# Kernel tuning notes

Hardware: AMD Instinct MI355X
Metric: run time of the kernel (lower is better)

## Reference

```python
import jax, jax.numpy as jnp
import numpy as np

EPS = 1e-5


def layer_norm(x, g, b):
    m = jnp.mean(x, axis=-1, keepdims=True)
    v = jnp.mean((x - m) ** 2, axis=-1, keepdims=True)
    return (x - m) / jnp.sqrt(v + EPS) * g + b


def rel_shift(x, klen):
    # x: [q, p, b, n] -> Transformer-XL relative shift -> [q, klen, b, n]
    q, p, b, n = x.shape
    x = jnp.reshape(x, (p, q, b, n))
    x = x[1:]
    x = jnp.reshape(x, (q, p - 1, b, n))
    return x[:, :klen]


def setup_inputs() -> dict:
    S, B, D, NH, DH, DF = 1024, 4, 1024, 16, 64, 4096
    key = jax.random.key(0)
    ks = jax.random.split(key, 16)
    w = 0.02  # scale random params for numerical sanity
    return {
        "src": jax.random.normal(ks[0], (S, B, D), jnp.float32),
        "pos_emb": jax.random.normal(ks[1], (S + 1, B, D), jnp.float32),
        "src_mask": jnp.zeros((S, S), dtype=bool),
        "qw": jax.random.normal(ks[2], (D, NH, DH), jnp.float32) * w,
        "kw": jax.random.normal(ks[3], (D, NH, DH), jnp.float32) * w,
        "vw": jax.random.normal(ks[4], (D, NH, DH), jnp.float32) * w,
        "rw": jax.random.normal(ks[5], (D, NH, DH), jnp.float32) * w,
        "ow": jax.random.normal(ks[6], (D, NH, DH), jnp.float32) * w,
        "r_w_bias": jax.random.normal(ks[7], (NH, DH), jnp.float32) * w,
        "r_r_bias": jax.random.normal(ks[8], (NH, DH), jnp.float32) * w,
        "w1": jax.random.normal(ks[9], (DF, D), jnp.float32) * w,
        "b1": jnp.zeros((DF,), jnp.float32),
        "w2": jax.random.normal(ks[10], (D, DF), jnp.float32) * w,
        "b2": jnp.zeros((D,), jnp.float32),
        "g1": jnp.ones((D,), jnp.float32),
        "beta1": jnp.zeros((D,), jnp.float32),
        "g2": jnp.ones((D,), jnp.float32),
        "beta2": jnp.zeros((D,), jnp.float32),
    }


def reference(src, pos_emb, src_mask, qw, kw, vw, rw, ow, r_w_bias, r_r_bias,
              w1, b1, w2, b2, g1, beta1, g2, beta2):
    S = src.shape[0]
    d_head = qw.shape[-1]
    scale = 1.0 / d_head ** 0.5

    # mem=None -> cat == src; dropout layers are identity (eval)
    q_head = jnp.einsum('ibh,hnd->ibnd', src, qw)
    k_head = jnp.einsum('ibh,hnd->ibnd', src, kw)
    v_head = jnp.einsum('ibh,hnd->ibnd', src, vw)
    k_pos = jnp.einsum('ibh,hnd->ibnd', pos_emb, rw)

    ac = jnp.einsum('ibnd,jbnd->ijbn', q_head + r_w_bias, k_head)       # [S,S,B,N]
    bd = jnp.einsum('ibnd,jbnd->ijbn', q_head + r_r_bias, k_pos)        # [S,S+1,B,N]
    bd = rel_shift(bd, klen=S)

    mask = src_mask.astype(ac.dtype)[:, :, None, None]
    attn_score = (ac + bd) * scale - 1e30 * mask
    attn_prob = jax.nn.softmax(attn_score, axis=1)

    attn_vec = jnp.einsum('ijbn,jbnd->ibnd', attn_prob, v_head)
    attn_out = jnp.einsum('ibnd,hnd->ibh', attn_vec, ow)

    x = layer_norm(src + attn_out, g1, beta1)
    ff = jax.nn.gelu(x @ w1.T + b1, approximate=False) @ w2.T + b2
    return layer_norm(x + ff, g2, beta2)
```

## Files before the change

### kernel.cpp

```cpp
#include <hip/hip_runtime.h>
#include <math.h>

typedef __bf16 bf16x8 __attribute__((ext_vector_type(8)));
typedef __bf16 bf16x4 __attribute__((ext_vector_type(4)));
typedef float f32x4 __attribute__((ext_vector_type(4)));

__device__ __forceinline__ void gload_lds16(const __bf16* g, __bf16* l) {
  __builtin_amdgcn_global_load_lds((const __attribute__((address_space(1))) void*)g,
                                   (__attribute__((address_space(3))) void*)l, 16, 0, 0);
}

__device__ __forceinline__ float gelu_exact(float v) {
  return 0.5f * v * (1.f + erff(v * 0.70710678118654752f));
}

__global__ __launch_bounds__(256) void prep_all(
    const float* __restrict__ src, __bf16* __restrict__ srcB2,
    const float* __restrict__ pos, __bf16* __restrict__ posB,
    const float* __restrict__ ow, __bf16* __restrict__ owB,
    const float* __restrict__ w1, __bf16* __restrict__ w1B,
    const float* __restrict__ w2, __bf16* __restrict__ w2B,
    const float* __restrict__ qw, const float* __restrict__ kw,
    const float* __restrict__ vw, const float* __restrict__ rw,
    __bf16* __restrict__ qkvT, __bf16* __restrict__ rwT) {
  __shared__ float t[32][33];
  int bid = blockIdx.x;
  const int tid = threadIdx.x;
  if (bid < 4096) {
    const int i = bid & 1023, b = bid >> 10;
    const float4 v = *(const float4*)(src + ((size_t)(i * 4 + b)) * 1024 + tid * 4);
    bf16x4 o = {(__bf16)v.x, (__bf16)v.y, (__bf16)v.z, (__bf16)v.w};
    *(bf16x4*)(srcB2 + (size_t)bid * 1024 + tid * 4) = o;
    return;
  }
  bid -= 4096;
  if (bid < 3329) {
    const float* in; __bf16* out;
    if (bid < 1025) { in = pos; out = posB; }
    else if (bid < 1281) { bid -= 1025; in = ow; out = owB; }
    else if (bid < 2305) { bid -= 1281; in = w1; out = w1B; }
    else { bid -= 2305; in = w2; out = w2B; }
    const int base = bid * 4096 + tid * 4;
#pragma unroll
    for (int k2 = 0; k2 < 4; ++k2) {
      const int off = base + k2 * 1024;
      float4 v = *(const float4*)(in + off);
      bf16x4 o = {(__bf16)v.x, (__bf16)v.y, (__bf16)v.z, (__bf16)v.w};
      *(bf16x4*)(out + off) = o;
    }
    return;
  }
  bid -= 3329;
  const int z = bid >> 10, rem = bid & 1023;
  const float* in; __bf16* out;
  switch (z) {
    case 0: in = qw; out = qkvT; break;
    case 1: in = kw; out = qkvT + 1024 * 1024; break;
    case 2: in = vw; out = qkvT + 2048 * 1024; break;
    default: in = rw; out = rwT; break;
  }
  const int c0 = (rem & 31) * 32, r0 = (rem >> 5) * 32;
  const int tx = tid & 31, ty = tid >> 5;
  for (int yy = ty; yy < 32; yy += 8)
    t[yy][tx] = in[(size_t)(r0 + yy) * 1024 + c0 + tx];
  __syncthreads();
  for (int yy = ty; yy < 32; yy += 8)
    out[(size_t)(c0 + yy) * 1024 + r0 + tx] = (__bf16)t[tx][yy];
}

template<int BM, int BN, int MODE>
__device__ __forceinline__ void gemm_body(
    const __bf16* __restrict__ A, const __bf16* __restrict__ BT,
    float* __restrict__ Cf, __bf16* __restrict__ Cb,
    const float* __restrict__ bias, int M, int N, int K,
    int kStart, int kChunk, int mBase, int nBase, char* smemRaw) {
  constexpr int BK = 32;
  constexpr int ALOAD = (BM * BK) / 2048;
  constexpr int BLOAD = (BN * BK) / 2048;
  __bf16* lA = (__bf16*)smemRaw;
  __bf16* lB = (__bf16*)(smemRaw + 4 * BM * BK);
  const int tid = threadIdx.x;
  const int w = tid >> 6, l = tid & 63;
  const int lr = l & 15, lk = l >> 4;
  const int srow = tid >> 2;
  const int scol = (tid & 3) * 8;
  const int wbase = w * 512;

  const __bf16* aSrc[ALOAD];
  const __bf16* bSrc[BLOAD];
#pragma unroll
  for (int i = 0; i < ALOAD; ++i) {
    int grow = mBase + srow + i * 64;
    grow = grow < M ? grow : M - 1;
    aSrc[i] = A + (size_t)grow * K + kStart + scol;
  }
#pragma unroll
  for (int i = 0; i < BLOAD; ++i) {
    const int grow = nBase + srow + i * 64;
    bSrc[i] = BT + (size_t)grow * K + kStart + scol;
  }
  auto stage = [&](int buf) {
#pragma unroll
    for (int i = 0; i < ALOAD; ++i) {
      gload_lds16(aSrc[i], &lA[buf * BM * BK + i * 2048 + wbase]);
      aSrc[i] += BK;
    }
#pragma unroll
    for (int i = 0; i < BLOAD; ++i) {
      gload_lds16(bSrc[i], &lB[buf * BN * BK + i * 2048 + wbase]);
      bSrc[i] += BK;
    }
  };

  constexpr int WM = BM / 2, WN = BN / 2;
  constexpr int MF = WM / 16, NF = WN / 16;
  const int wr = w >> 1, wc = w & 1;
  f32x4 acc[MF][NF] = {};

  const int nIter = kChunk / BK;
  stage(0);
  int cur = 0;
#pragma unroll 1
  for (int t = 0; t < nIter; ++t) {
    __syncthreads();
    if (t + 1 < nIter) stage(cur ^ 1);
    bf16x8 af[MF], bfr[NF];
#pragma unroll
    for (int mi = 0; mi < MF; ++mi)
      af[mi] = *(const bf16x8*)&lA[cur * BM * BK + (wr * WM + mi * 16 + lr) * BK + lk * 8];
#pragma unroll
    for (int nj = 0; nj < NF; ++nj)
      bfr[nj] = *(const bf16x8*)&lB[cur * BN * BK + (wc * WN + nj * 16 + lr) * BK + lk * 8];
#pragma unroll
    for (int mi = 0; mi < MF; ++mi)
#pragma unroll
      for (int nj = 0; nj < NF; ++nj)
        acc[mi][nj] = __builtin_amdgcn_mfma_f32_16x16x32_bf16(af[mi], bfr[nj], acc[mi][nj], 0, 0, 0);
    cur ^= 1;
  }
#pragma unroll
  for (int mi = 0; mi < MF; ++mi) {
#pragma unroll
    for (int nj = 0; nj < NF; ++nj) {
      const int col = nBase + wc * WN + nj * 16 + lr;
      const int row0 = mBase + wr * WM + mi * 16 + lk * 4;
#pragma unroll
      for (int j = 0; j < 4; ++j) {
        const int row = row0 + j;
        if (row < M) {
          float v = acc[mi][nj][j];
          if constexpr (MODE == 1) {
            v = gelu_exact(v + bias[col]);
            Cb[(size_t)row * N + col] = (__bf16)v;
          } else if constexpr (MODE == 2) {
            Cb[(size_t)row * N + col] = (__bf16)v;
          } else {
            Cf[(size_t)row * N + col] = v;
          }
        }
      }
    }
  }
}

__global__ __launch_bounds__(256)
void proj2_kernel(const __bf16* __restrict__ vwT, const __bf16* __restrict__ srcB2,
                  const __bf16* __restrict__ posB, const __bf16* __restrict__ rwT,
                  __bf16* __restrict__ vTB, __bf16* __restrict__ kposB) {
  __shared__ __align__(16) char smem[4 * (128 + 64) * 32];
  const int raw = blockIdx.x;
  int bid = (raw & 7) * 130 + (raw >> 3);
  if (bid < 512) {
    gemm_body<128, 64, 2>(vwT, srcB2, nullptr, vTB, nullptr, 1024, 4096, 1024,
                          0, 1024, (bid >> 6) * 128, (bid & 63) * 64, smem);
  } else {
    const int t = bid - 512;
    gemm_body<128, 64, 2>(posB, rwT, nullptr, kposB, nullptr, 4100, 1024, 1024,
                          0, 1024, (t >> 4) * 128, (t & 15) * 64, smem);
  }
}

template<int MODE>
__global__ __launch_bounds__(512)
void gemm256(const __bf16* __restrict__ A, const __bf16* __restrict__ BT,
             __bf16* __restrict__ Cb, const float* __restrict__ bias,
             int M, int N, int K) {
  __shared__ __align__(16) __bf16 sm[3 * 24576];
  const int tid = threadIdx.x;
  const int wid = tid >> 6, l = tid & 63;
  const int lcol = l & 15, lk = l >> 4;
  const int wm = wid >> 1, wn = wid & 1;
  const int gx = gridDim.x;
  const int G = gx * gridDim.y;
  const int flat = blockIdx.y * gx + blockIdx.x;
  const int band = G >> 3;
  const int x8 = flat & 7, loc = flat >> 3;
  const int rpb = band / gx;
  const int ny = x8 * rpb + loc % rpb;
  const int nx = loc / rpb;
  const int mBase = ny * 256, nBase = nx * 128;

  int rowj[2], gslotj[2];
#pragma unroll
  for (int j = 0; j < 2; ++j) {
    const int u = (wid * 2 + j) * 64 + l;
    rowj[j] = u >> 3;
    gslotj[j] = (u & 7) ^ (rowj[j] & 7);
  }
  auto issueHT = [&](int kt, int ht, int side) {
    __bf16* base = sm + side * 24576 + (ht == 2 ? 16384 : ht * 8192);
#pragma unroll
    for (int j = 0; j < 2; ++j) {
      const __bf16* src = (ht < 2)
        ? A + (size_t)(mBase + ht * 128 + rowj[j]) * K + kt * 64 + gslotj[j] * 8
        : BT + (size_t)(nBase + rowj[j]) * K + kt * 64 + gslotj[j] * 8;
      gload_lds16(src, base + (wid * 2 + j) * 512);
    }
  };

  const int nkt = K >> 6;
  issueHT(0, 0, 0); issueHT(0, 1, 0); issueHT(0, 2, 0);
  issueHT(1, 0, 1); issueHT(1, 1, 1); issueHT(1, 2, 1);

  f32x4 acc[4][4] = {};
#pragma unroll 1
  for (int j = 0; j < nkt; ++j) {
    asm volatile("s_waitcnt vmcnt(6)" ::: "memory");
    __builtin_amdgcn_s_barrier();
    __builtin_amdgcn_sched_barrier(0);
    const int side = j % 3;
    const int sn = (j + 2) % 3;
    const int ktn = (j + 2 < nkt) ? j + 2 : nkt - 1;
    const __bf16* Ab = sm + side * 24576;
    const __bf16* Bb = Ab + 16384;
    issueHT(ktn, 0, sn);
    bf16x8 af[4][2];
#pragma unroll
    for (int mi = 0; mi < 4; ++mi)
#pragma unroll
      for (int kk = 0; kk < 2; ++kk) {
        const int row = wm * 64 + mi * 16 + lcol;
        af[mi][kk] = *(const bf16x8*)&Ab[row * 64 + (((kk * 4 + lk) ^ (row & 7)) * 8)];
      }
    issueHT(ktn, 1, sn);
    bf16x8 bfv[4][2];
#pragma unroll
    for (int nj = 0; nj < 4; ++nj)
#pragma unroll
      for (int kk = 0; kk < 2; ++kk) {
        const int row = wn * 64 + nj * 16 + lcol;
        bfv[nj][kk] = *(const bf16x8*)&Bb[row * 64 + (((kk * 4 + lk) ^ (row & 7)) * 8)];
      }
    issueHT(ktn, 2, sn);
    __builtin_amdgcn_s_setprio(1);
#pragma unroll
    for (int mi = 0; mi < 4; ++mi)
#pragma unroll
      for (int nj = 0; nj < 4; ++nj) {
        acc[mi][nj] = __builtin_amdgcn_mfma_f32_16x16x32_bf16(af[mi][0], bfv[nj][0], acc[mi][nj], 0, 0, 0);
        acc[mi][nj] = __builtin_amdgcn_mfma_f32_16x16x32_bf16(af[mi][1], bfv[nj][1], acc[mi][nj], 0, 0, 0);
      }
    __builtin_amdgcn_s_setprio(0);
  }
#pragma unroll
  for (int mi = 0; mi < 4; ++mi)
#pragma unroll
    for (int nj = 0; nj < 4; ++nj) {
      const int col = nBase + wn * 64 + nj * 16 + lcol;
      const int row0 = mBase + wm * 64 + mi * 16 + lk * 4;
#pragma unroll
      for (int jj = 0; jj < 4; ++jj) {
        float v = acc[mi][nj][jj];
        if constexpr (MODE == 1) v = gelu_exact(v + bias[col]);
        Cb[(size_t)(row0 + jj) * N + col] = (__bf16)v;
      }
    }
}

template<int MODE>
__global__ __launch_bounds__(512)
void gemm512(const __bf16* __restrict__ A, const __bf16* __restrict__ BT,
             __bf16* __restrict__ Cb0, __bf16* __restrict__ Cb1,
             __bf16* __restrict__ Cb2, __bf16* __restrict__ Cb3,
             const float* __restrict__ bias, int M, int N, int K, int kChunk) {
  __shared__ __align__(16) __bf16 sm[2 * 32768];
  const int tid = threadIdx.x;
  const int w = tid >> 6, l = tid & 63;
  const int lcol = l & 15, lk = l >> 4;
  const int wm = w >> 2, wn = w & 3;
  const int gx = gridDim.x;
  const int G = gx * gridDim.y;
  const int flat = blockIdx.y * gx + blockIdx.x;
  const int band = G >> 3;
  const int x8 = flat & 7, loc = flat >> 3;
  const int rpb = band / gx;
  const int ny = x8 * rpb + loc % rpb;
  const int nx = loc / rpb;
  const int mBase = ny * 256, nBase = nx * 256;
  const int kStart = blockIdx.z * kChunk;
  __bf16* Cb = (blockIdx.z == 0) ? Cb0 : (blockIdx.z == 1) ? Cb1
             : (blockIdx.z == 2) ? Cb2 : Cb3;

  const int rT = tid >> 3;
  const int gslot = ((tid & 7) ^ (rT & 7)) * 8;
  auto stage = [&](int side, int kt) {
#pragma unroll
    for (int i = 0; i < 4; ++i) {
      gload_lds16(A + (size_t)(mBase + i * 64 + rT) * K + kStart + kt * 64 + gslot,
                  sm + side * 32768 + i * 4096 + w * 512);
      gload_lds16(BT + (size_t)(nBase + i * 64 + rT) * K + kStart + kt * 64 + gslot,
                  sm + side * 32768 + 16384 + i * 4096 + w * 512);
    }
  };

  f32x4 acc[8][4] = {};
  const int nIter = kChunk >> 6;
  stage(0, 0);
  int cur = 0;
#pragma unroll 1
  for (int t = 0; t < nIter; ++t) {
    __syncthreads();
    if (t + 1 < nIter) stage(cur ^ 1, t + 1);
    const __bf16* Ab = sm + cur * 32768;
    const __bf16* Bb = Ab + 16384;
    bf16x8 bfv[4][2];
#pragma unroll
    for (int nj = 0; nj < 4; ++nj)
#pragma unroll
      for (int kk = 0; kk < 2; ++kk) {
        const int row = wn * 64 + nj * 16 + lcol;
        bfv[nj][kk] = *(const bf16x8*)&Bb[row * 64 + (((kk * 4 + lk) ^ (row & 7)) * 8)];
      }
    __builtin_amdgcn_s_setprio(1);
#pragma unroll
    for (int mi = 0; mi < 8; ++mi) {
      const int row = wm * 128 + mi * 16 + lcol;
      bf16x8 a0 = *(const bf16x8*)&Ab[row * 64 + ((lk ^ (row & 7)) * 8)];
      bf16x8 a1 = *(const bf16x8*)&Ab[row * 64 + (((4 + lk) ^ (row & 7)) * 8)];
#pragma unroll
      for (int nj = 0; nj < 4; ++nj) {
        acc[mi][nj] = __builtin_amdgcn_mfma_f32_16x16x32_bf16(a0, bfv[nj][0], acc[mi][nj], 0, 0, 0);
        acc[mi][nj] = __builtin_amdgcn_mfma_f32_16x16x32_bf16(a1, bfv[nj][1], acc[mi][nj], 0, 0, 0);
      }
    }
    __builtin_amdgcn_s_setprio(0);
    cur ^= 1;
  }
#pragma unroll
  for (int mi = 0; mi < 8; ++mi)
#pragma unroll
    for (int nj = 0; nj < 4; ++nj) {
      const int col = nBase + wn * 64 + nj * 16 + lcol;
      const int row0 = mBase + wm * 128 + mi * 16 + lk * 4;
#pragma unroll
      for (int jj = 0; jj < 4; ++jj) {
        float v = acc[mi][nj][jj];
        if constexpr (MODE == 1) v = gelu_exact(v + bias[col]);
        Cb[(size_t)(row0 + jj) * N + col] = (__bf16)v;
      }
    }
}

__global__ __launch_bounds__(256)
void attn10(const __bf16* __restrict__ qk, const __bf16* __restrict__ vT,
            const __bf16* __restrict__ kpos, const float* __restrict__ rwbias,
            const float* __restrict__ rrbias, __bf16* __restrict__ av) {
  constexpr float ALPHA = 0.125f * 1.44269504088896f;
  constexpr int PB = 132;
  __shared__ __align__(16) char smem[74240];
  __bf16* sP  = (__bf16*)(smem + 49152);
  __bf16* sbd = (__bf16*)(smem + 57344);

  const int flat = blockIdx.x;
  const int xcd = flat & 7, rr_ = flat >> 3;
  const int bn = xcd * 8 + (rr_ >> 4);
  const int it = rr_ & 15;
  const int b = bn >> 4, n = bn & 15;
  const int i0 = it * 64;
  const int tid = threadIdx.x;
  const int l = tid & 63;
  const int lcol = l & 15, lk = l >> 4;
  const int strip = (tid >> 6) * 16;
  const int wbase = tid & 192;
  const int nh64 = n * 64;
  const int q = strip + lcol;

  const int rB = tid >> 3;
  const int cs8 = ((tid & 7) ^ (rB & 7)) * 8;

  bf16x8 onesf;
#pragma unroll
  for (int u = 0; u < 8; ++u) onesf[u] = (__bf16)1.0f;

  bf16x8 qac[2], qlo[2], qhi[2];
  {
    const __bf16* qrow = qk + ((size_t)(b * 1024 + i0 + q)) * 2048 + nh64;
    int gH = i0 + q + 1; gH = gH < 1024 ? gH : 1023;
    const __bf16* qrowH = qk + ((size_t)(b * 1024 + gH)) * 2048 + nh64;
#pragma unroll
    for (int kk = 0; kk < 2; ++kk) {
      bf16x8 qv = *(const bf16x8*)(qrow + kk * 32 + lk * 8);
      bf16x8 qh = *(const bf16x8*)(qrowH + kk * 32 + lk * 8);
      const int dbase = nh64 + kk * 32 + lk * 8;
#pragma unroll
      for (int u = 0; u < 8; ++u) {
        const float rb = rrbias[dbase + u];
        qac[kk][u] = (__bf16)(((float)qv[u] + rwbias[dbase + u]) * ALPHA);
        qlo[kk][u] = (__bf16)(((float)qv[u] + rb) * ALPHA);
        qhi[kk][u] = (__bf16)(((float)qh[u] + rb) * ALPHA);
      }
    }
  }

#pragma unroll
  for (int kq = 0; kq < 2; ++kq) {
    const int r = kq * 32 + rB;
    const int dst = (kq * 256 + wbase) * 8;
    gload_lds16(kpos + ((size_t)((960 - i0 + r) * 4 + b)) * 1024 + nh64 + cs8,
                (__bf16*)(smem + 40960) + dst);
    gload_lds16(qk + ((size_t)(b * 1024 + r)) * 2048 + 1024 + nh64 + cs8,
                (__bf16*)(smem) + dst);
    const int rrel = r - i0;
    const int idx = (rrel <= 0) ? (1024 + rrel) : (rrel - 1);
    gload_lds16(kpos + ((size_t)(idx * 4 + b)) * 1024 + nh64 + cs8,
                (__bf16*)(smem + 16384) + dst);
    gload_lds16(vT + ((size_t)(nh64 + r)) * 4096 + b * 1024 + cs8,
                (__bf16*)(smem + 32768) + dst);
  }
  __syncthreads();
  {
    __bf16* kpl = (__bf16*)(smem + 40960);
    const int colb0 = (-i0 - 64) & 127;
#pragma unroll
    for (int fb = 0; fb < 4; ++fb) {
      const int row = fb * 16 + lcol;
      f32x4 g = {};
#pragma unroll
      for (int kk = 0; kk < 2; ++kk) {
        bf16x8 a = *(const bf16x8*)&kpl[row * 64 + (((kk * 4 + lk) ^ (lcol & 7)) * 8)];
        g = __builtin_amdgcn_mfma_f32_16x16x32_bf16(a, qlo[kk], g, 0, 0, 0);
      }
      bf16x4 gw = {(__bf16)g[0], (__bf16)g[1], (__bf16)g[2], (__bf16)g[3]};
      *(bf16x4*)&sbd[q * PB + ((colb0 + fb * 16 + lk * 4) & 127)] = gw;
    }
  }
  __syncthreads();

  f32x4 oacc[4] = {};
  f32x4 zq = {};
  size_t kS = (size_t)(b * 1024 + 64 + rB) * 2048 + 1024 + nh64 + cs8;
  size_t vS = (size_t)(nh64 + rB) * 4096 + b * 1024 + 64 + cs8;

  auto jtStep = [&](int jt, const bf16x8 (&qg)[2], bool dofix) {
    const int cur = jt & 1, nxt = cur ^ 1;
    const int d0 = jt * 64 - i0;
    __bf16* sK   = (__bf16*)(smem + cur * 8192);
    __bf16* sKn  = (__bf16*)(smem + nxt * 8192);
    __bf16* sKP  = (__bf16*)(smem + 16384 + cur * 8192);
    __bf16* sKPn = (__bf16*)(smem + 16384 + nxt * 8192);
    __bf16* sVT  = (__bf16*)(smem + 32768 + cur * 8192);
    __bf16* sVTn = (__bf16*)(smem + 32768 + nxt * 8192);
#pragma unroll
    for (int kq = 0; kq < 2; ++kq) {
      const int dst = (kq * 256 + wbase) * 8;
      gload_lds16(qk + kS + kq * 65536, sKn + dst);
      gload_lds16(vT + vS + kq * 131072, sVTn + dst);
      const int rreln = d0 + 64 + kq * 32 + rB;
      const int idx = (rreln <= 0) ? (1024 + rreln) : (rreln - 1);
      gload_lds16(kpos + ((size_t)(idx * 4 + b)) * 1024 + nh64 + cs8, sKPn + dst);
    }
    kS += 131072; vS += 64;
    {
      __builtin_amdgcn_s_setprio(1);
#pragma unroll
      for (int fb = 0; fb < 4; ++fb) {
        const int row = fb * 16 + lcol;
        f32x4 g = {};
        g = __builtin_amdgcn_mfma_f32_16x16x32_bf16(
            *(const bf16x8*)&sKP[row * 64 + ((lk ^ (lcol & 7)) * 8)], qg[0], g, 0, 0, 0);
        g = __builtin_amdgcn_mfma_f32_16x16x32_bf16(
            *(const bf16x8*)&sKP[row * 64 + (((4 + lk) ^ (lcol & 7)) * 8)], qg[1], g, 0, 0, 0);
        bf16x4 gw = {(__bf16)g[0], (__bf16)g[1], (__bf16)g[2], (__bf16)g[3]};
        *(bf16x4*)&sbd[q * PB + ((d0 + fb * 16 + lk * 4) & 127)] = gw;
      }
      __builtin_amdgcn_s_setprio(0);
      if (dofix) {
        const int cl = tid >> 2, part = tid & 3;
        const __bf16* qs = qk + ((size_t)(b * 1024 + i0 + cl)) * 2048 + nh64 + part * 16;
        bf16x8 a0 = *(const bf16x8*)qs;
        bf16x8 a1 = *(const bf16x8*)(qs + 8);
        bf16x8 k0 = *(const bf16x8*)&sKP[(2 * part) * 8];
        bf16x8 k1 = *(const bf16x8*)&sKP[(2 * part + 1) * 8];
        float s64 = 0.f;
#pragma unroll
        for (int u = 0; u < 8; ++u)
          s64 += ((float)a0[u] + rrbias[nh64 + part * 16 + u]) * (float)k0[u]
               + ((float)a1[u] + rrbias[nh64 + part * 16 + 8 + u]) * (float)k1[u];
        s64 += __shfl_xor(s64, 1, 64);
        s64 += __shfl_xor(s64, 2, 64);
        if (part == 0) sbd[cl * PB] = (__bf16)(s64 * ALPHA);
      }
    }
    f32x4 sc[4];
    __builtin_amdgcn_s_setprio(1);
#pragma unroll
    for (int fk = 0; fk < 4; ++fk) {
      const int row = fk * 16 + lcol;
      f32x4 a = {};
#pragma unroll
      for (int kk = 0; kk < 2; ++kk) {
        bf16x8 kf = *(const bf16x8*)&sK[row * 64 + (((kk * 4 + lk) ^ (lcol & 7)) * 8)];
        a = __builtin_amdgcn_mfma_f32_16x16x32_bf16(kf, qac[kk], a, 0, 0, 0);
      }
      sc[fk] = a;
    }
    __builtin_amdgcn_s_setprio(0);
    {
      const int rowb = q * PB;
      const int sb = d0 - q;
#pragma unroll
      for (int fk = 0; fk < 4; ++fk) {
        const int cb = sb + fk * 16 + lk * 4;
        float e0 = exp2f(sc[fk][0] + (float)sbd[rowb + ((cb) & 127)]);
        float e1 = exp2f(sc[fk][1] + (float)sbd[rowb + ((cb + 1) & 127)]);
        float e2 = exp2f(sc[fk][2] + (float)sbd[rowb + ((cb + 2) & 127)]);
        float e3 = exp2f(sc[fk][3] + (float)sbd[rowb + ((cb + 3) & 127)]);
        bf16x4 pw = {(__bf16)e0, (__bf16)e1, (__bf16)e2, (__bf16)e3};
        *(bf16x4*)&sP[q * 64 + (((fk * 2 + (lk >> 1)) ^ (q & 7)) * 8) + (lk & 1) * 4] = pw;
      }
    }
    __builtin_amdgcn_s_setprio(1);
#pragma unroll
    for (int kk = 0; kk < 2; ++kk) {
      bf16x8 pa = *(const bf16x8*)&sP[q * 64 + (((kk * 4 + lk) ^ (q & 7)) * 8)];
      zq = __builtin_amdgcn_mfma_f32_16x16x32_bf16(pa, onesf, zq, 0, 0, 0);
#pragma unroll
      for (int fd = 0; fd < 4; ++fd) {
        const int vrow = fd * 16 + lcol;
        bf16x8 bv = *(const bf16x8*)&sVT[vrow * 64 + (((kk * 4 + lk) ^ (lcol & 7)) * 8)];
        oacc[fd] = __builtin_amdgcn_mfma_f32_16x16x32_bf16(pa, bv, oacc[fd], 0, 0, 0);
      }
    }
    __builtin_amdgcn_s_setprio(0);
    __syncthreads();
  };

#pragma unroll 1
  for (int jt = 0; jt < it; ++jt) jtStep(jt, qlo, false);
  jtStep(it, qhi, true);
#pragma unroll 1
  for (int jt = it + 1; jt < 16; ++jt) jtStep(jt, qhi, false);

#pragma unroll
  for (int jj = 0; jj < 4; ++jj) {
    const float rz = 1.f / zq[jj];
    const int ig = i0 + strip + lk * 4 + jj;
    __bf16* dst = av + ((size_t)(ig * 4 + b)) * 1024 + nh64;
#pragma unroll
    for (int fd = 0; fd < 4; ++fd)
      dst[fd * 16 + lcol] = (__bf16)(oacc[fd][jj] * rz);
  }
}

__global__ __launch_bounds__(256)
void ln_fuse(const float* __restrict__ A, const __bf16* __restrict__ Ab,
             const __bf16* __restrict__ P0, const __bf16* __restrict__ P1,
             const __bf16* __restrict__ P2, const __bf16* __restrict__ P3,
             const float* __restrict__ cb, const float* __restrict__ g,
             const float* __restrict__ be, float* __restrict__ oF,
             __bf16* __restrict__ oB) {
  const int row = blockIdx.x, t = threadIdx.x;
  const size_t base = (size_t)row * 1024 + t * 4;
  float x0, x1, x2, x3;
  if (A) {
    const float4 a = *(const float4*)(A + base);
    x0 = a.x; x1 = a.y; x2 = a.z; x3 = a.w;
  } else {
    const bf16x4 a = *(const bf16x4*)(Ab + base);
    x0 = (float)a[0]; x1 = (float)a[1]; x2 = (float)a[2]; x3 = (float)a[3];
  }
  const bf16x4 p0 = *(const bf16x4*)(P0 + base);
  const bf16x4 p1 = *(const bf16x4*)(P1 + base);
  const bf16x4 p2 = *(const bf16x4*)(P2 + base);
  const bf16x4 p3 = *(const bf16x4*)(P3 + base);
  x0 += (float)p0[0] + (float)p1[0] + (float)p2[0] + (float)p3[0];
  x1 += (float)p0[1] + (float)p1[1] + (float)p2[1] + (float)p3[1];
  x2 += (float)p0[2] + (float)p1[2] + (float)p2[2] + (float)p3[2];
  x3 += (float)p0[3] + (float)p1[3] + (float)p2[3] + (float)p3[3];
  if (cb) {
    const float4 c = *(const float4*)(cb + t * 4);
    x0 += c.x; x1 += c.y; x2 += c.z; x3 += c.w;
  }
  float s = x0 + x1 + x2 + x3;
  float qq = x0 * x0 + x1 * x1 + x2 * x2 + x3 * x3;
#pragma unroll
  for (int o = 1; o < 64; o <<= 1) { s += __shfl_xor(s, o, 64); qq += __shfl_xor(qq, o, 64); }
  __shared__ float ss[4], qs[4];
  if ((t & 63) == 0) { ss[t >> 6] = s; qs[t >> 6] = qq; }
  __syncthreads();
  s = ss[0] + ss[1] + ss[2] + ss[3];
  qq = qs[0] + qs[1] + qs[2] + qs[3];
  const float mean = s * (1.f / 1024.f);
  const float var = qq * (1.f / 1024.f) - mean * mean;
  const float rstd = rsqrtf(var + 1e-5f);
  const float4 gv = *(const float4*)(g + t * 4);
  const float4 bev = *(const float4*)(be + t * 4);
  const float y0 = (x0 - mean) * rstd * gv.x + bev.x;
  const float y1 = (x1 - mean) * rstd * gv.y + bev.y;
  const float y2 = (x2 - mean) * rstd * gv.z + bev.z;
  const float y3 = (x3 - mean) * rstd * gv.w + bev.w;
  if (oF) {
    float4 r = {y0, y1, y2, y3};
    *(float4*)(oF + base) = r;
  }
  if (oB) {
    bf16x4 o4 = {(__bf16)y0, (__bf16)y1, (__bf16)y2, (__bf16)y3};
    *(bf16x4*)(oB + base) = o4;
  }
}

extern "C" void kernel_launch(void* const* d_in, const int* in_sizes, int n_in,
                              void* d_out, int out_size, void* d_ws, size_t ws_size,
                              hipStream_t stream) {
  const float* src    = (const float*)d_in[0];
  const float* pos    = (const float*)d_in[1];
  const float* qw     = (const float*)d_in[3];
  const float* kw     = (const float*)d_in[4];
  const float* vw     = (const float*)d_in[5];
  const float* rw     = (const float*)d_in[6];
  const float* ow     = (const float*)d_in[7];
  const float* rwbias = (const float*)d_in[8];
  const float* rrbias = (const float*)d_in[9];
  const float* w1     = (const float*)d_in[10];
  const float* b1     = (const float*)d_in[11];
  const float* w2     = (const float*)d_in[12];
  const float* b2     = (const float*)d_in[13];
  const float* g1     = (const float*)d_in[14];
  const float* be1    = (const float*)d_in[15];
  const float* g2     = (const float*)d_in[16];
  const float* be2    = (const float*)d_in[17];
  float* out = (float*)d_out;

  char* p = (char*)d_ws;
  auto alloc = [&](size_t bytes) { char* r = p; p += (bytes + 255) & ~(size_t)255; return r; };
  __bf16* qkB   = (__bf16*)alloc(4096ull * 2048 * 2);
  __bf16* vTB   = (__bf16*)alloc(1024ull * 4096 * 2);
  __bf16* kposB = (__bf16*)alloc(4100ull * 1024 * 2);
  __bf16* avB   = (__bf16*)alloc(4096ull * 1024 * 2);
  __bf16* srcB2 = (__bf16*)alloc(4096ull * 1024 * 2);
  __bf16* posB  = (__bf16*)alloc(4100ull * 1024 * 2);
  float*  xF    = (float*)alloc(4096ull * 1024 * 4);
  __bf16* w2B   = (__bf16*)alloc(4096ull * 1024 * 2);
  __bf16* qkvT  = (__bf16*)alloc(3072ull * 1024 * 2);
  __bf16* rwT   = (__bf16*)alloc(1024ull * 1024 * 2);
  __bf16* owB   = (__bf16*)alloc(1024ull * 1024 * 2);
  __bf16* w1B   = (__bf16*)alloc(4096ull * 1024 * 2);
  __bf16* xB    = (__bf16*)alloc(4096ull * 1024 * 2);
  __bf16* gB   = qkB;
  __bf16* xS0  = (__bf16*)xF;
  __bf16* xS1  = (__bf16*)xF + 4194304;

  prep_all<<<11521, 256, 0, stream>>>(src, srcB2, pos, posB, ow, owB, w1, w1B,
                                      w2, w2B, qw, kw, vw, rw, qkvT, rwT);
  gemm256<2><<<dim3(16, 16), 512, 0, stream>>>(srcB2, qkvT, qkB, nullptr, 4096, 2048, 1024);
  proj2_kernel<<<1040, 256, 0, stream>>>(qkvT + 2048 * 1024, srcB2, posB, rwT, vTB, kposB);
  attn10<<<dim3(1024), 256, 0, stream>>>(qkB, vTB, kposB, rwbias, rrbias, avB);
  gemm512<2><<<dim3(4, 16, 4), 512, 0, stream>>>(avB, owB, srcB2, posB, xS0, xS1, nullptr, 4096, 1024, 1024, 256);
  ln_fuse<<<4096, 256, 0, stream>>>(src, nullptr, srcB2, posB, xS0, xS1, nullptr, g1, be1, nullptr, xB);
  gemm512<1><<<dim3(16, 16), 512, 0, stream>>>(xB, w1B, gB, nullptr, nullptr, nullptr, b1, 4096, 4096, 1024, 1024);
  gemm512<2><<<dim3(4, 16, 4), 512, 0, stream>>>(gB, w2B, avB, w1B, xS0, xS1, nullptr, 4096, 1024, 4096, 1024);
  ln_fuse<<<4096, 256, 0, stream>>>(nullptr, xB, avB, w1B, xS0, xS1, b2, g2, be2, out, nullptr);
  (void)in_sizes; (void)n_in; (void)out_size; (void)ws_size;
}
```

Before: 285.2 us.

## Replace double-buffered LDS prefetch in attention with register-staged single buffer

The attention kernel no longer double-buffers its K, positional-K and V^T tiles in LDS using direct global-to-LDS loads. It now prefetches the next tile into registers during the current step, then writes it into a single LDS buffer after an extra barrier. This cuts static LDS from about 74 KB to about 49 KB, which could allow more resident blocks per CU. In exchange it adds a second __syncthreads per iteration, extra VGPR pressure and explicit LDS store instructions.

```diff
diff --git a/kernel.cpp b/kernel.cpp
--- a/kernel.cpp
+++ b/kernel.cpp
@@ -362,14 +362,17 @@
 }
 
 __global__ __launch_bounds__(256)
-void attn10(const __bf16* __restrict__ qk, const __bf16* __restrict__ vT,
+void attn11(const __bf16* __restrict__ qk, const __bf16* __restrict__ vT,
             const __bf16* __restrict__ kpos, const float* __restrict__ rwbias,
             const float* __restrict__ rrbias, __bf16* __restrict__ av) {
   constexpr float ALPHA = 0.125f * 1.44269504088896f;
   constexpr int PB = 132;
-  __shared__ __align__(16) char smem[74240];
-  __bf16* sP  = (__bf16*)(smem + 49152);
-  __bf16* sbd = (__bf16*)(smem + 57344);
+  __shared__ __align__(16) char smem[49664];
+  __bf16* sK  = (__bf16*)(smem);
+  __bf16* sKP = (__bf16*)(smem + 8192);
+  __bf16* sVT = (__bf16*)(smem + 16384);
+  __bf16* sP  = (__bf16*)(smem + 24576);
+  __bf16* sbd = (__bf16*)(smem + 32768);
 
   const int flat = blockIdx.x;
   const int xcd = flat & 7, rr_ = flat >> 3;
@@ -416,20 +419,16 @@
   for (int kq = 0; kq < 2; ++kq) {
     const int r = kq * 32 + rB;
     const int dst = (kq * 256 + wbase) * 8;
-    gload_lds16(kpos + ((size_t)((960 - i0 + r) * 4 + b)) * 1024 + nh64 + cs8,
-                (__bf16*)(smem + 40960) + dst);
-    gload_lds16(qk + ((size_t)(b * 1024 + r)) * 2048 + 1024 + nh64 + cs8,
-                (__bf16*)(smem) + dst);
+    gload_lds16(kpos + ((size_t)((960 - i0 + r) * 4 + b)) * 1024 + nh64 + cs8, sP + dst);
+    gload_lds16(qk + ((size_t)(b * 1024 + r)) * 2048 + 1024 + nh64 + cs8, sK + dst);
     const int rrel = r - i0;
     const int idx = (rrel <= 0) ? (1024 + rrel) : (rrel - 1);
-    gload_lds16(kpos + ((size_t)(idx * 4 + b)) * 1024 + nh64 + cs8,
-                (__bf16*)(smem + 16384) + dst);
-    gload_lds16(vT + ((size_t)(nh64 + r)) * 4096 + b * 1024 + cs8,
-                (__bf16*)(smem + 32768) + dst);
+    gload_lds16(kpos + ((size_t)(idx * 4 + b)) * 1024 + nh64 + cs8, sKP + dst);
+    gload_lds16(vT + ((size_t)(nh64 + r)) * 4096 + b * 1024 + cs8, sVT + dst);
   }
   __syncthreads();
   {
-    __bf16* kpl = (__bf16*)(smem + 40960);
+    const __bf16* kpl = sP;
     const int colb0 = (-i0 - 64) & 127;
 #pragma unroll
     for (int fb = 0; fb < 4; ++fb) {
@@ -452,22 +451,15 @@
   size_t vS = (size_t)(nh64 + rB) * 4096 + b * 1024 + 64 + cs8;
 
   auto jtStep = [&](int jt, const bf16x8 (&qg)[2], bool dofix) {
-    const int cur = jt & 1, nxt = cur ^ 1;
     const int d0 = jt * 64 - i0;
-    __bf16* sK   = (__bf16*)(smem + cur * 8192);
-    __bf16* sKn  = (__bf16*)(smem + nxt * 8192);
-    __bf16* sKP  = (__bf16*)(smem + 16384 + cur * 8192);
-    __bf16* sKPn = (__bf16*)(smem + 16384 + nxt * 8192);
-    __bf16* sVT  = (__bf16*)(smem + 32768 + cur * 8192);
-    __bf16* sVTn = (__bf16*)(smem + 32768 + nxt * 8192);
+    bf16x8 rKr[2], rKPr[2], rVTr[2];
 #pragma unroll
     for (int kq = 0; kq < 2; ++kq) {
-      const int dst = (kq * 256 + wbase) * 8;
-      gload_lds16(qk + kS + kq * 65536, sKn + dst);
-      gload_lds16(vT + vS + kq * 131072, sVTn + dst);
+      rKr[kq] = *(const bf16x8*)(qk + kS + kq * 65536);
+      rVTr[kq] = *(const bf16x8*)(vT + vS + kq * 131072);
       const int rreln = d0 + 64 + kq * 32 + rB;
       const int idx = (rreln <= 0) ? (1024 + rreln) : (rreln - 1);
-      gload_lds16(kpos + ((size_t)(idx * 4 + b)) * 1024 + nh64 + cs8, sKPn + dst);
+      rKPr[kq] = *(const bf16x8*)(kpos + ((size_t)(idx * 4 + b)) * 1024 + nh64 + cs8);
     }
     kS += 131072; vS += 64;
     {
@@ -542,6 +534,14 @@
       }
     }
     __builtin_amdgcn_s_setprio(0);
+    __syncthreads();
+#pragma unroll
+    for (int kq = 0; kq < 2; ++kq) {
+      const int dst = (kq * 256 + tid) * 8;
+      *(bf16x8*)(sK + dst) = rKr[kq];
+      *(bf16x8*)(sKP + dst) = rKPr[kq];
+      *(bf16x8*)(sVT + dst) = rVTr[kq];
+    }
     __syncthreads();
   };
 
@@ -664,7 +664,7 @@
                                       w2, w2B, qw, kw, vw, rw, qkvT, rwT);
   gemm256<2><<<dim3(16, 16), 512, 0, stream>>>(srcB2, qkvT, qkB, nullptr, 4096, 2048, 1024);
   proj2_kernel<<<1040, 256, 0, stream>>>(qkvT + 2048 * 1024, srcB2, posB, rwT, vTB, kposB);
-  attn10<<<dim3(1024), 256, 0, stream>>>(qkB, vTB, kposB, rwbias, rrbias, avB);
+  attn11<<<dim3(1024), 256, 0, stream>>>(qkB, vTB, kposB, rwbias, rrbias, avB);
   gemm512<2><<<dim3(4, 16, 4), 512, 0, stream>>>(avB, owB, srcB2, posB, xS0, xS1, nullptr, 4096, 1024, 1024, 256);
   ln_fuse<<<4096, 256, 0, stream>>>(src, nullptr, srcB2, posB, xS0, xS1, nullptr, g1, be1, nullptr, xB);
   gemm512<1><<<dim3(16, 16), 512, 0, stream>>>(xB, w1B, gB, nullptr, nullptr, nullptr, b1, 4096, 4096, 1024, 1024);
```

Result: no change. 284.4 us, median of 2 (-0.3%).
